# Kernel optimization log

Hardware: AMD Instinct MI355X
Metric: run time of the kernel (lower is better)

## Reference

```python
import jax, jax.numpy as jnp
import numpy as np

B, N, D_IN, D_OUT = 16, 2048, 512, 512


def setup_inputs() -> dict:
    key = jax.random.key(0)
    ks = jax.random.split(key, 7)
    s = 1.0 / np.sqrt(D_IN)
    return {
        "x": jax.random.normal(ks[0], (B, N, D_IN), dtype=jnp.float32),
        "Wq": jax.random.uniform(ks[1], (D_IN, D_OUT), jnp.float32, -s, s),
        "bq": jax.random.uniform(ks[2], (D_OUT,), jnp.float32, -s, s),
        "Wk": jax.random.uniform(ks[3], (D_IN, D_OUT), jnp.float32, -s, s),
        "bk": jax.random.uniform(ks[4], (D_OUT,), jnp.float32, -s, s),
        "Wv": jax.random.uniform(ks[5], (D_IN, D_OUT), jnp.float32, -s, s),
        "bv": jax.random.uniform(ks[6], (D_OUT,), jnp.float32, -s, s),
    }


def reference(x, Wq, bq, Wk, bk, Wv, bv):
    # Q/K/V projections: [B,N,D]
    q = jnp.einsum("bnd,de->bne", x, Wq) + bq
    k = jnp.einsum("bnd,de->bne", x, Wk) + bk
    v = jnp.einsum("bnd,de->bne", x, Wv) + bv
    # Full NxN attention, no scaling (faithful to the original module)
    scores = jnp.einsum("bqe,bke->bqk", q, k)
    attn = jax.nn.softmax(scores, axis=-1)
    return jnp.einsum("bqk,bke->bqe", attn, v)
```

## Files before the change

kernel.cpp:

```cpp
#include <hip/hip_runtime.h>

typedef _Float16 half8  __attribute__((ext_vector_type(8)));
typedef _Float16 half4_t __attribute__((ext_vector_type(4)));
typedef float    f32x4  __attribute__((ext_vector_type(4)));

static constexpr int BATCH = 16;
static constexpr int NSEQ  = 2048;
static constexpr int DDIM  = 512;
static constexpr int MROWS = BATCH * NSEQ;

static constexpr size_t WT_OFF  = 0;
static constexpr size_t QKV_OFF = 2u * 1024 * 1024;
static constexpr size_t VT_OFF  = QKV_OFF + (size_t)3 * MROWS * DDIM * 2;

typedef const __attribute__((address_space(1))) void cg_void;
typedef __attribute__((address_space(3))) void lds_void;
__device__ __forceinline__ void gload_lds16(const void* g, void* l) {
    __builtin_amdgcn_global_load_lds((cg_void*)g, (lds_void*)l, 16, 0, 0);
}

__global__ void xconv(const float* __restrict__ x, _Float16* __restrict__ xh) {
    size_t base = ((size_t)blockIdx.x * 256 + threadIdx.x) * 8;
    float4 a = *(const float4*)(x + base);
    float4 b = *(const float4*)(x + base + 4);
    half8 h;
    h[0] = (_Float16)a.x; h[1] = (_Float16)a.y; h[2] = (_Float16)a.z; h[3] = (_Float16)a.w;
    h[4] = (_Float16)b.x; h[5] = (_Float16)b.y; h[6] = (_Float16)b.z; h[7] = (_Float16)b.w;
    *(half8*)(xh + base) = h;
}

__global__ void wt_prep(const float* __restrict__ Wq, const float* __restrict__ Wk,
                        const float* __restrict__ Wv, _Float16* __restrict__ wt) {
    int idx = blockIdx.x * 256 + threadIdx.x;
    int ng  = idx >> 9;
    int e   = idx & 511;
    const float* W = (ng < 512) ? Wq : (ng < 1024 ? Wk : Wv);
    wt[idx] = (_Float16)W[e * 512 + (ng & 511)];
}

__global__ __launch_bounds__(256, 2) void qkv_gemm(
        const _Float16* __restrict__ xh, const _Float16* __restrict__ wt,
        const float* __restrict__ bq, const float* __restrict__ bk,
        const float* __restrict__ bv, _Float16* __restrict__ qkv) {
    __shared__ alignas(16) char Asw[128 * 128];
    __shared__ alignas(16) char Bsw[128 * 128];
    const int tid  = threadIdx.x;
    const int lane = tid & 63;
    const int wid  = tid >> 6;
    const int lg = lane >> 4, lm = lane & 15;
    const int wr = wid >> 1, wc = wid & 1;

    const int id = blockIdx.x;
    const int wg = (id & 7) * 384 + (id >> 3);
    const int bm = wg & 255, bn = wg >> 8;
    const int m0 = bm * 128, n0 = bn * 128;
    const int proj = n0 >> 9;
    const float* bias = (proj == 0) ? bq : (proj == 1 ? bk : bv);

    f32x4 acc[4][4] = {};

    const int rloc = (lane >> 3);
    const int p    = lane & 7;

    for (int kk = 0; kk < 512; kk += 64) {
        __syncthreads();
        #pragma unroll
        for (int i = 0; i < 4; ++i) {
            int g = wid * 4 + i;
            int r = g * 8 + rloc;
            gload_lds16(xh + (size_t)(m0 + r) * 512 + kk + ((p ^ (r & 7)) * 8),
                        Asw + g * 1024);
            gload_lds16(wt + (size_t)(n0 + r) * 512 + kk + ((p ^ (r & 7)) * 8),
                        Bsw + g * 1024);
        }
        __syncthreads();
        #pragma unroll
        for (int es = 0; es < 2; ++es) {
            half8 a[4], b[4];
            #pragma unroll
            for (int i = 0; i < 4; ++i) {
                int row = wr * 64 + i * 16 + lm;
                a[i] = *(const half8*)(Asw + row * 128 + (((es * 4 + lg) ^ (row & 7)) * 16));
            }
            #pragma unroll
            for (int j = 0; j < 4; ++j) {
                int row = wc * 64 + j * 16 + lm;
                b[j] = *(const half8*)(Bsw + row * 128 + (((es * 4 + lg) ^ (row & 7)) * 16));
            }
            #pragma unroll
            for (int i = 0; i < 4; ++i)
                #pragma unroll
                for (int j = 0; j < 4; ++j)
                    acc[i][j] = __builtin_amdgcn_mfma_f32_16x16x32_f16(a[i], b[j], acc[i][j], 0, 0, 0);
        }
    }
    const size_t pb = (size_t)proj * MROWS * DDIM;
    #pragma unroll
    for (int i = 0; i < 4; ++i) {
        #pragma unroll
        for (int j = 0; j < 4; ++j) {
            int mg = m0 + wr * 64 + i * 16 + lg * 4;
            int c  = (n0 & 511) + wc * 64 + j * 16 + lm;
            float bb = bias[c];
            #pragma unroll
            for (int r = 0; r < 4; ++r)
                qkv[pb + (size_t)(mg + r) * DDIM + c] = (_Float16)(acc[i][j][r] + bb);
        }
    }
}

__global__ void v_transpose(const _Float16* __restrict__ v, _Float16* __restrict__ vt) {
    __shared__ alignas(16) _Float16 T[64][72];
    const int b = blockIdx.z;
    const int n0 = blockIdx.x * 64, e0 = blockIdx.y * 64;
    const int tid = threadIdx.x;
    #pragma unroll
    for (int i = 0; i < 2; ++i) {
        int c = tid + i * 256;
        int row = c >> 3, o = c & 7;
        int4 val = *(const int4*)(v + ((size_t)b * NSEQ + n0 + row) * 512 + e0 + o * 8);
        *(int4*)&T[row][o * 8] = val;
    }
    __syncthreads();
    #pragma unroll
    for (int i = 0; i < 2; ++i) {
        int c = tid + i * 256;
        int erow = c >> 3, o = c & 7;
        _Float16 tmp[8];
        #pragma unroll
        for (int j = 0; j < 8; ++j) tmp[j] = T[o * 8 + j][erow];
        *(int4*)(vt + (size_t)b * 512 * NSEQ + (size_t)(e0 + erow) * NSEQ + n0 + o * 8) =
            *(int4*)tmp;
    }
}

__global__ __launch_bounds__(512, 2) void attn(
        const _Float16* __restrict__ q, const _Float16* __restrict__ k,
        const _Float16* __restrict__ vt, float* __restrict__ out) {
    __shared__ alignas(16) char KsB[2 * 32768];
    __shared__ alignas(16) char VsB[2 * 32768];
    __shared__ alignas(16) _Float16 Pl[8][16][40];

    const int tid = threadIdx.x, lane = tid & 63, wid = tid >> 6;
    const int lg = lane >> 4, lm = lane & 15;

    const int id = blockIdx.x;
    const int b  = (id & 7) | ((id >> 7) << 3);
    const int n0 = ((id >> 3) & 15) * 128;

    const _Float16* qrow = q + ((size_t)(b * NSEQ + n0 + wid * 16 + lm)) * 512;
    half8 qf[16];
    #pragma unroll
    for (int es = 0; es < 16; ++es)
        qf[es] = *(const half8*)(qrow + es * 32 + lg * 8);

    f32x4 o[32] = {};
    float m_r[4], l_r[4];
    #pragma unroll
    for (int r = 0; r < 4; ++r) { m_r[r] = -__builtin_inff(); l_r[r] = 0.f; }

    const _Float16* kb  = k  + (size_t)b * NSEQ * 512;
    const _Float16* vtb = vt + (size_t)b * 512 * NSEQ;

    int koff[4], voff[4];
    #pragma unroll
    for (int i = 0; i < 4; ++i) {
        int R = wid * 4 + i;
        koff[i] = R * 512 + ((lane ^ (R & 7)) * 8);
        voff[i] = (R * 16 + (lane >> 2)) * NSEQ + (((lane & 3) ^ ((lane >> 3) & 3)) * 8);
    }

    auto STAGE = [&](int tt, int bb) {
        const _Float16* ks = kb + (size_t)tt * (32 * 512);
        const _Float16* vs = vtb + (size_t)tt * 32;
        #pragma unroll
        for (int i = 0; i < 4; ++i) {
            gload_lds16(ks + koff[i], KsB + bb * 32768 + (wid * 4 + i) * 1024);
            gload_lds16(vs + voff[i], VsB + bb * 32768 + (wid * 4 + i) * 1024);
        }
    };

    STAGE(0, 0);
    STAGE(1, 1);

    for (int t = 0; t < 64; ++t) {
        if (t < 62) asm volatile("s_waitcnt vmcnt(8)" ::: "memory");
        else        asm volatile("s_waitcnt vmcnt(0)" ::: "memory");
        __builtin_amdgcn_s_barrier();

        const char* Ksb = KsB + (t & 1) * 32768;
        const char* Vsb = VsB + (t & 1) * 32768;

        f32x4 s0 = {}, s1 = {};
        __builtin_amdgcn_s_setprio(1);
        #pragma unroll
        for (int es = 0; es < 16; ++es) {
            const int off = es * 64 + lg * 16;
            half8 k0 = *(const half8*)(Ksb + lm * 1024 + (off ^ ((lm & 7) << 4)));
            half8 k1 = *(const half8*)(Ksb + (lm + 16) * 1024 + (off ^ ((lm & 7) << 4)));
            s0 = __builtin_amdgcn_mfma_f32_16x16x32_f16(qf[es], k0, s0, 0, 0, 0);
            s1 = __builtin_amdgcn_mfma_f32_16x16x32_f16(qf[es], k1, s1, 0, 0, 0);
        }
        __builtin_amdgcn_s_setprio(0);

        float sc[4], p0[4], p1[4];
        bool resc = false;
        #pragma unroll
        for (int r = 0; r < 4; ++r) {
            float tm = fmaxf(s0[r], s1[r]);
            #pragma unroll
            for (int d = 1; d < 16; d <<= 1) tm = fmaxf(tm, __shfl_xor(tm, d));
            float mn = fmaxf(m_r[r], tm);
            float use_m;
            if (mn - m_r[r] <= 8.f) {
                use_m = m_r[r]; sc[r] = 1.f;
            } else {
                use_m = mn; sc[r] = __expf(m_r[r] - mn); m_r[r] = mn; resc = true;
            }
            p0[r] = __expf(s0[r] - use_m);
            p1[r] = __expf(s1[r] - use_m);
            float rsum = p0[r] + p1[r];
            #pragma unroll
            for (int d = 1; d < 16; d <<= 1) rsum += __shfl_xor(rsum, d);
            l_r[r] = l_r[r] * sc[r] + rsum;
        }

        #pragma unroll
        for (int r = 0; r < 4; ++r) {
            Pl[wid][lg * 4 + r][lm]      = (_Float16)p0[r];
            Pl[wid][lg * 4 + r][lm + 16] = (_Float16)p1[r];
        }
        half8 pf = *(const half8*)&Pl[wid][lm][lg * 8];

        if (__any((int)resc)) {
            #pragma unroll
            for (int eg = 0; eg < 32; ++eg)
                #pragma unroll
                for (int r = 0; r < 4; ++r) o[eg][r] *= sc[r];
        }

        __builtin_amdgcn_s_setprio(1);
        #pragma unroll
        for (int eg = 0; eg < 32; ++eg) {
            int e = eg * 16 + lm;
            half8 vf = *(const half8*)(Vsb + e * 64 + ((lg ^ ((lm >> 1) & 3)) << 4));
            o[eg] = __builtin_amdgcn_mfma_f32_16x16x32_f16(pf, vf, o[eg], 0, 0, 0);
        }
        __builtin_amdgcn_s_setprio(0);

        __builtin_amdgcn_s_barrier();
        asm volatile("" ::: "memory");
        if (t + 2 < 64) STAGE(t + 2, t & 1);
    }

    float inv[4];
    #pragma unroll
    for (int r = 0; r < 4; ++r) inv[r] = 1.f / l_r[r];
    float* ob = out + ((size_t)(b * NSEQ + n0 + wid * 16 + lg * 4)) * 512;
    #pragma unroll
    for (int eg = 0; eg < 32; ++eg)
        #pragma unroll
        for (int r = 0; r < 4; ++r)
            ob[(size_t)r * 512 + eg * 16 + lm] = o[eg][r] * inv[r];
}

extern "C" void kernel_launch(void* const* d_in, const int* in_sizes, int n_in,
                              void* d_out, int out_size, void* d_ws, size_t ws_size,
                              hipStream_t stream) {
    const float* x  = (const float*)d_in[0];
    const float* Wq = (const float*)d_in[1];
    const float* bq = (const float*)d_in[2];
    const float* Wk = (const float*)d_in[3];
    const float* bk = (const float*)d_in[4];
    const float* Wv = (const float*)d_in[5];
    const float* bv = (const float*)d_in[6];
    float* out = (float*)d_out;
    char* ws = (char*)d_ws;

    _Float16* wt   = (_Float16*)(ws + WT_OFF);
    _Float16* qkv  = (_Float16*)(ws + QKV_OFF);
    _Float16* qbuf = qkv;
    _Float16* kbuf = qkv + (size_t)1 * MROWS * DDIM;
    _Float16* vbuf = qkv + (size_t)2 * MROWS * DDIM;
    _Float16* vt   = (_Float16*)(ws + VT_OFF);
    _Float16* xh   = (_Float16*)(ws + VT_OFF);

    xconv<<<8192, 256, 0, stream>>>(x, xh);
    wt_prep<<<(1536 * 512) / 256, 256, 0, stream>>>(Wq, Wk, Wv, wt);
    qkv_gemm<<<3072, 256, 0, stream>>>(xh, wt, bq, bk, bv, qkv);
    v_transpose<<<dim3(NSEQ / 64, DDIM / 64, BATCH), 256, 0, stream>>>(vbuf, vt);
    attn<<<256, 512, 0, stream>>>(qbuf, kbuf, vt, out);
}
```

Measured before the change: 528.9 us.

## Double-buffer QKV GEMM loads and transpose score MFMA for cheaper softmax reductions

The QKV GEMM now uses two LDS buffers and issues the next k-slice load before computing on the current one, so global-to-LDS traffic overlaps MFMA work instead of sitting behind a barrier. In attention, the score MFMA operands are swapped so each lane holds one query row. That turns the row max and sum into two cross-lane shuffles instead of four per row, with one scalar m/l state per lane. The attention prefetch drops from two tiles ahead to one with __syncthreads instead of explicit vmcnt waits, and the s_setprio hints are removed, which may expose more load latency. The P tile padding changes to 48 to suit the new vectorized half4 stores.

```diff
diff --git a/kernel.cpp b/kernel.cpp
--- a/kernel.cpp
+++ b/kernel.cpp
@@ -42,8 +42,8 @@
         const _Float16* __restrict__ xh, const _Float16* __restrict__ wt,
         const float* __restrict__ bq, const float* __restrict__ bk,
         const float* __restrict__ bv, _Float16* __restrict__ qkv) {
-    __shared__ alignas(16) char Asw[128 * 128];
-    __shared__ alignas(16) char Bsw[128 * 128];
+    __shared__ alignas(16) char Asw[2][128 * 128];
+    __shared__ alignas(16) char Bsw[2][128 * 128];
     const int tid  = threadIdx.x;
     const int lane = tid & 63;
     const int wid  = tid >> 6;
@@ -62,30 +62,36 @@
     const int rloc = (lane >> 3);
     const int p    = lane & 7;
 
-    for (int kk = 0; kk < 512; kk += 64) {
-        __syncthreads();
+    auto STAGE = [&](int kk, int bb) {
         #pragma unroll
         for (int i = 0; i < 4; ++i) {
             int g = wid * 4 + i;
             int r = g * 8 + rloc;
             gload_lds16(xh + (size_t)(m0 + r) * 512 + kk + ((p ^ (r & 7)) * 8),
-                        Asw + g * 1024);
+                        Asw[bb] + g * 1024);
             gload_lds16(wt + (size_t)(n0 + r) * 512 + kk + ((p ^ (r & 7)) * 8),
-                        Bsw + g * 1024);
-        }
+                        Bsw[bb] + g * 1024);
+        }
+    };
+
+    STAGE(0, 0);
+    for (int ks = 0; ks < 8; ++ks) {
         __syncthreads();
+        if (ks < 7) STAGE((ks + 1) * 64, (ks & 1) ^ 1);
+        const char* Ab = Asw[ks & 1];
+        const char* Bb = Bsw[ks & 1];
         #pragma unroll
         for (int es = 0; es < 2; ++es) {
             half8 a[4], b[4];
             #pragma unroll
             for (int i = 0; i < 4; ++i) {
                 int row = wr * 64 + i * 16 + lm;
-                a[i] = *(const half8*)(Asw + row * 128 + (((es * 4 + lg) ^ (row & 7)) * 16));
+                a[i] = *(const half8*)(Ab + row * 128 + (((es * 4 + lg) ^ (row & 7)) * 16));
             }
             #pragma unroll
             for (int j = 0; j < 4; ++j) {
                 int row = wc * 64 + j * 16 + lm;
-                b[j] = *(const half8*)(Bsw + row * 128 + (((es * 4 + lg) ^ (row & 7)) * 16));
+                b[j] = *(const half8*)(Bb + row * 128 + (((es * 4 + lg) ^ (row & 7)) * 16));
             }
             #pragma unroll
             for (int i = 0; i < 4; ++i)
@@ -139,7 +145,7 @@
         const _Float16* __restrict__ vt, float* __restrict__ out) {
     __shared__ alignas(16) char KsB[2 * 32768];
     __shared__ alignas(16) char VsB[2 * 32768];
-    __shared__ alignas(16) _Float16 Pl[8][16][40];
+    __shared__ alignas(16) _Float16 Pl[8][16][48];
 
     const int tid = threadIdx.x, lane = tid & 63, wid = tid >> 6;
     const int lg = lane >> 4, lm = lane & 15;
@@ -155,9 +161,7 @@
         qf[es] = *(const half8*)(qrow + es * 32 + lg * 8);
 
     f32x4 o[32] = {};
-    float m_r[4], l_r[4];
-    #pragma unroll
-    for (int r = 0; r < 4; ++r) { m_r[r] = -__builtin_inff(); l_r[r] = 0.f; }
+    float m_r = -__builtin_inff(), l_r = 0.f;
 
     const _Float16* kb  = k  + (size_t)b * NSEQ * 512;
     const _Float16* vtb = vt + (size_t)b * 512 * NSEQ;
@@ -181,81 +185,72 @@
     };
 
     STAGE(0, 0);
-    STAGE(1, 1);
-
     for (int t = 0; t < 64; ++t) {
-        if (t < 62) asm volatile("s_waitcnt vmcnt(8)" ::: "memory");
-        else        asm volatile("s_waitcnt vmcnt(0)" ::: "memory");
-        __builtin_amdgcn_s_barrier();
-
+        __syncthreads();
+        if (t < 63) STAGE(t + 1, (t & 1) ^ 1);
         const char* Ksb = KsB + (t & 1) * 32768;
         const char* Vsb = VsB + (t & 1) * 32768;
 
         f32x4 s0 = {}, s1 = {};
-        __builtin_amdgcn_s_setprio(1);
         #pragma unroll
         for (int es = 0; es < 16; ++es) {
             const int off = es * 64 + lg * 16;
             half8 k0 = *(const half8*)(Ksb + lm * 1024 + (off ^ ((lm & 7) << 4)));
             half8 k1 = *(const half8*)(Ksb + (lm + 16) * 1024 + (off ^ ((lm & 7) << 4)));
-            s0 = __builtin_amdgcn_mfma_f32_16x16x32_f16(qf[es], k0, s0, 0, 0, 0);
-            s1 = __builtin_amdgcn_mfma_f32_16x16x32_f16(qf[es], k1, s1, 0, 0, 0);
-        }
-        __builtin_amdgcn_s_setprio(0);
-
-        float sc[4], p0[4], p1[4];
-        bool resc = false;
+            s0 = __builtin_amdgcn_mfma_f32_16x16x32_f16(k0, qf[es], s0, 0, 0, 0);
+            s1 = __builtin_amdgcn_mfma_f32_16x16x32_f16(k1, qf[es], s1, 0, 0, 0);
+        }
+
+        float tm = fmaxf(fmaxf(fmaxf(s0[0], s0[1]), fmaxf(s0[2], s0[3])),
+                         fmaxf(fmaxf(s1[0], s1[1]), fmaxf(s1[2], s1[3])));
+        tm = fmaxf(tm, __shfl_xor(tm, 16));
+        tm = fmaxf(tm, __shfl_xor(tm, 32));
+        float mn = fmaxf(m_r, tm);
+        const bool skip = __all((int)(mn - m_r <= 8.f));
+        float use_m, sc;
+        if (skip) { use_m = m_r; sc = 1.f; }
+        else      { use_m = mn; sc = __expf(m_r - mn); m_r = mn; }
+
+        float p0[4], p1[4];
         #pragma unroll
         for (int r = 0; r < 4; ++r) {
-            float tm = fmaxf(s0[r], s1[r]);
-            #pragma unroll
-            for (int d = 1; d < 16; d <<= 1) tm = fmaxf(tm, __shfl_xor(tm, d));
-            float mn = fmaxf(m_r[r], tm);
-            float use_m;
-            if (mn - m_r[r] <= 8.f) {
-                use_m = m_r[r]; sc[r] = 1.f;
-            } else {
-                use_m = mn; sc[r] = __expf(m_r[r] - mn); m_r[r] = mn; resc = true;
-            }
             p0[r] = __expf(s0[r] - use_m);
             p1[r] = __expf(s1[r] - use_m);
-            float rsum = p0[r] + p1[r];
-            #pragma unroll
-            for (int d = 1; d < 16; d <<= 1) rsum += __shfl_xor(rsum, d);
-            l_r[r] = l_r[r] * sc[r] + rsum;
-        }
-
-        #pragma unroll
-        for (int r = 0; r < 4; ++r) {
-            Pl[wid][lg * 4 + r][lm]      = (_Float16)p0[r];
-            Pl[wid][lg * 4 + r][lm + 16] = (_Float16)p1[r];
-        }
+        }
+        float rsum = (p0[0] + p0[1]) + (p0[2] + p0[3]) +
+                     (p1[0] + p1[1]) + (p1[2] + p1[3]);
+        rsum += __shfl_xor(rsum, 16);
+        rsum += __shfl_xor(rsum, 32);
+        l_r = l_r * sc + rsum;
+
+        half4_t h0, h1;
+        #pragma unroll
+        for (int r = 0; r < 4; ++r) { h0[r] = (_Float16)p0[r]; h1[r] = (_Float16)p1[r]; }
+        *(half4_t*)&Pl[wid][lm][lg * 4]      = h0;
+        *(half4_t*)&Pl[wid][lm][16 + lg * 4] = h1;
         half8 pf = *(const half8*)&Pl[wid][lm][lg * 8];
 
-        if (__any((int)resc)) {
+        if (!skip) {
+            float scq[4];
+            #pragma unroll
+            for (int r = 0; r < 4; ++r) scq[r] = __shfl(sc, lg * 4 + r);
             #pragma unroll
             for (int eg = 0; eg < 32; ++eg)
                 #pragma unroll
-                for (int r = 0; r < 4; ++r) o[eg][r] *= sc[r];
-        }
-
-        __builtin_amdgcn_s_setprio(1);
+                for (int r = 0; r < 4; ++r) o[eg][r] *= scq[r];
+        }
+
         #pragma unroll
         for (int eg = 0; eg < 32; ++eg) {
             int e = eg * 16 + lm;
             half8 vf = *(const half8*)(Vsb + e * 64 + ((lg ^ ((lm >> 1) & 3)) << 4));
             o[eg] = __builtin_amdgcn_mfma_f32_16x16x32_f16(pf, vf, o[eg], 0, 0, 0);
         }
-        __builtin_amdgcn_s_setprio(0);
-
-        __builtin_amdgcn_s_barrier();
-        asm volatile("" ::: "memory");
-        if (t + 2 < 64) STAGE(t + 2, t & 1);
     }
 
     float inv[4];
     #pragma unroll
-    for (int r = 0; r < 4; ++r) inv[r] = 1.f / l_r[r];
+    for (int r = 0; r < 4; ++r) inv[r] = 1.f / __shfl(l_r, lg * 4 + r);
     float* ob = out + ((size_t)(b * NSEQ + n0 + wid * 16 + lg * 4)) * 512;
     #pragma unroll
     for (int eg = 0; eg < 32; ++eg)
```

Result: faster. 440.6 us (-16.7%).
